# Optimization experiments

Measured on AMD Instinct MI355X. Metric: run time of the kernel, lower is better.

The kernel has to match this reference:

```python
import jax, jax.numpy as jnp
import numpy as np

UNITS = 512
INPUT_SIZE = 512
BATCH = 64
SEQ_LEN = 512


def setup_inputs() -> dict:
    key = jax.random.key(0)
    k_x, k_wx, k_wh = jax.random.split(key, 3)
    scale_x = 1.0 / np.sqrt(INPUT_SIZE)
    scale_h = 1.0 / np.sqrt(UNITS)
    return {
        "x": jax.random.normal(k_x, (BATCH, SEQ_LEN, INPUT_SIZE), dtype=jnp.float32),
        "h0": jnp.zeros((BATCH, UNITS), dtype=jnp.float32),
        "c0": jnp.zeros((BATCH, UNITS), dtype=jnp.float32),
        "Wx": jax.random.normal(k_wx, (INPUT_SIZE, 4 * UNITS), dtype=jnp.float32) * scale_x,
        "Wh": jax.random.normal(k_wh, (UNITS, 4 * UNITS), dtype=jnp.float32) * scale_h,
        "b": jnp.zeros((4 * UNITS,), dtype=jnp.float32),
    }


def reference(x, h0, c0, Wx, Wh, b):
    """LSTM layer over full sequence; returns stacked hidden states [seq_len, batch, units]
    (matching TensorArray.stack() time-major output of the original)."""

    def step(carry, xt):
        h, c = carry
        # fused gate pre-activations: [batch, 4*units]
        z = xt @ Wx + h @ Wh + b
        i, f, g, o = jnp.split(z, 4, axis=-1)  # Keras gate order: i, f, c(g), o
        i = jax.nn.sigmoid(i)
        f = jax.nn.sigmoid(f)
        g = jnp.tanh(g)
        o = jax.nn.sigmoid(o)
        c_new = f * c + i * g
        h_new = o * jnp.tanh(c_new)
        return (h_new, c_new), h_new

    xs = jnp.swapaxes(x, 0, 1)  # [seq_len, batch, input_size]
    (_, _), hs = jax.lax.scan(step, (h0, c0), xs)
    return hs  # [seq_len, batch, units]
```

## Files before the change

### kernel.cpp

```cpp
#include <hip/hip_runtime.h>
#include <stdint.h>


#define OFF_XBF   0ull
#define OFF_HL    33554432ull
#define OFF_HG    33816576ull

typedef short short8 __attribute__((ext_vector_type(8)));
typedef float f32x4 __attribute__((ext_vector_type(4)));
typedef unsigned u32x4 __attribute__((ext_vector_type(4)));

__device__ __forceinline__ unsigned f32_to_bf16(float f) {
    union { float f; unsigned u; } v; v.f = f;
    unsigned u = v.u;
    unsigned r = u + 0x7FFFu + ((u >> 16) & 1u);
    return r >> 16;
}

__global__ void prep_kernel(const float* __restrict__ x,
                            const float* __restrict__ h0,
                            unsigned char* __restrict__ ws) {
    long long i = (long long)blockIdx.x * blockDim.x + threadIdx.x;
    if (i < 2097152) {
        const float4* xs = (const float4*)x + i * 2;
        float4 a = xs[0], b = xs[1];
        unsigned w0 = f32_to_bf16(a.x) | (f32_to_bf16(a.y) << 16);
        unsigned w1 = f32_to_bf16(a.z) | (f32_to_bf16(a.w) << 16);
        unsigned w2 = f32_to_bf16(b.x) | (f32_to_bf16(b.y) << 16);
        unsigned w3 = f32_to_bf16(b.z) | (f32_to_bf16(b.w) << 16);
        uint4 o; o.x = w0; o.y = w1; o.z = w2; o.w = w3;
        ((uint4*)(ws + OFF_XBF))[i] = o;
        return;
    }
    i -= 2097152;
    if (i < 16384) {
        int b = (int)(i >> 8), p = (int)(i & 255);
        unsigned lo = f32_to_bf16(h0[b * 512 + 2 * p]);
        unsigned hi = f32_to_bf16(h0[b * 512 + 2 * p + 1]);
        unsigned long long v =
            (unsigned long long)(lo | (hi << 16)) | (1ull << 32);
        ((unsigned long long*)(ws + OFF_HL))[(long long)b * 256 + p] = v;
        ((unsigned long long*)(ws + OFF_HG))[(long long)b * 256 + p] = v;
    }
}

#define POLL_ONCE(BASEPTR, CPOL, TAGV, OKV, H0V, H1V)                          \
    {                                                                          \
        u32x4 p0, p1, p2, p3;                                                  \
        asm volatile(                                                          \
            "global_load_dwordx4 %0, %4, off " CPOL "\n\t"                     \
            "global_load_dwordx4 %1, %4, off offset:16 " CPOL "\n\t"           \
            "global_load_dwordx4 %2, %4, off offset:32 " CPOL "\n\t"           \
            "global_load_dwordx4 %3, %4, off offset:48 " CPOL "\n\t"           \
            "s_waitcnt vmcnt(0)"                                               \
            : "=v"(p0), "=v"(p1), "=v"(p2), "=v"(p3)                           \
            : "v"(BASEPTR)                                                     \
            : "memory");                                                       \
        unsigned bad = (p0.y ^ (TAGV)) | (p0.w ^ (TAGV))                       \
                     | (p1.y ^ (TAGV)) | (p1.w ^ (TAGV))                       \
                     | (p2.y ^ (TAGV)) | (p2.w ^ (TAGV))                       \
                     | (p3.y ^ (TAGV)) | (p3.w ^ (TAGV));                      \
        OKV = (bad == 0u);                                                     \
        if (OKV) {                                                             \
            H0V.x = p0.x; H0V.y = p0.z; H0V.z = p1.x; H0V.w = p1.z;            \
            H1V.x = p2.x; H1V.y = p2.z; H1V.z = p3.x; H1V.w = p3.z;            \
        }                                                                      \
    }

#define SPIN_DUAL(LPTR, GPTR, TAGV, H0V, H1V)                                  \
    {                                                                          \
        int ok_ = 0, it_ = 0;                                                  \
        for (;;) {                                                             \
            POLL_ONCE(LPTR, "sc0", TAGV, ok_, H0V, H1V);                       \
            if (ok_) break;                                                    \
            if ((it_ & 7) == 7) {                                              \
                POLL_ONCE(GPTR, "sc0 sc1", TAGV, ok_, H0V, H1V);               \
                if (ok_) break;                                                \
            }                                                                  \
            ++it_;                                                             \
            __builtin_amdgcn_s_sleep(0);                                       \
        }                                                                      \
    }

__launch_bounds__(256, 1)
__global__ void lstm_kernel(const float* __restrict__ c0,
                            const float* __restrict__ bias,
                            const float* __restrict__ Wx,
                            const float* __restrict__ Wh,
                            float* __restrict__ out,
                            unsigned char* __restrict__ ws) {
    const int tid  = threadIdx.x;
    const int bid  = blockIdx.x;
    const int s    = bid & 7;
    const int jg   = bid >> 3;
    const int lane = tid & 63;
    const int wave = tid >> 6;
    const int nl   = lane & 15;
    const int q    = lane >> 4;
    const int up   = nl & 3;
    const int g    = nl >> 2;

    const unsigned short* xbf = (const unsigned short*)(ws + OFF_XBF);
    unsigned long long* HuL = (unsigned long long*)(ws + OFF_HL);
    unsigned long long* HuG = (unsigned long long*)(ws + OFF_HG);

    __shared__ __align__(16) unsigned char lds[20736];
    float* lds_out = (float*)(lds + 16640);

    const int ncol = g * 512 + jg * 16 + wave * 4 + up;
    short8 fWh[16], fWx[16];
#pragma unroll
    for (int kt = 0; kt < 16; ++kt) {
        const int k0 = kt * 32 + q * 8;
        short8 vh, vx;
#pragma unroll
        for (int j = 0; j < 8; ++j) {
            vh[j] = (short)f32_to_bf16(Wh[(long long)(k0 + j) * 2048 + ncol]);
            vx[j] = (short)f32_to_bf16(Wx[(long long)(k0 + j) * 2048 + ncol]);
        }
        fWh[kt] = vh; fWx[kt] = vx;
    }

    const int ub = jg * 16 + wave * 4 + up;
    const float bi  = bias[ub];
    const float bf_ = bias[512 + ub];
    const float bg  = bias[1024 + ub];
    const float bo  = bias[1536 + ub];

    float cr[4];
#pragma unroll
    for (int r = 0; r < 4; ++r) {
        const int m = q * 4 + r;
        cr[r] = (q < 2) ? c0[(8 * s + m) * 512 + ub] : 0.f;
    }

    const int sm = tid >> 5, sc = tid & 31;
    const int sb = 8 * s + sm;
    const unsigned* xsrc_base = (const unsigned*)xbf + (long long)sb * 131072 + sc * 8;
    const unsigned char* hl_base = (const unsigned char*)(HuL + sb * 256 + sc * 8);
    const unsigned char* hg_base = (const unsigned char*)(HuG + sb * 256 + sc * 8);
    uint4* xdst = (uint4*)(lds + sm * 1040 + sc * 32);
    uint4* hdst = (uint4*)(lds + 8320 + sm * 1040 + sc * 32);

    const unsigned char* axp = lds + nl * 1040 + q * 16;
    const unsigned char* ahp = lds + 8320 + nl * 1040 + q * 16;
    const short8 zfrag = {0, 0, 0, 0, 0, 0, 0, 0};

    const int gbase = (lane & 0x30) | (lane & 3);
    const int sl0 = gbase, sl1 = gbase | 4, sl2 = gbase | 8, sl3 = gbase | 12;

    uint4 px0 = *(const uint4*)(xsrc_base);
    uint4 px1 = *(const uint4*)(xsrc_base + 4);
    xdst[0] = px0; xdst[1] = px1;
    px0 = *(const uint4*)(xsrc_base + 256);
    px1 = *(const uint4*)(xsrc_base + 256 + 4);
    __syncthreads();

    f32x4 accx;
    {
        f32x4 a0 = {0.f,0.f,0.f,0.f}, a1 = {0.f,0.f,0.f,0.f};
#pragma unroll
        for (int kt = 0; kt < 16; kt += 2) {
            short8 v0 = (nl < 8) ? *(const short8*)(axp + kt * 64) : zfrag;
            short8 v1 = (nl < 8) ? *(const short8*)(axp + kt * 64 + 64) : zfrag;
            a0 = __builtin_amdgcn_mfma_f32_16x16x32_bf16(v0, fWx[kt], a0, 0, 0, 0);
            a1 = __builtin_amdgcn_mfma_f32_16x16x32_bf16(v1, fWx[kt + 1], a1, 0, 0, 0);
        }
        accx = a0 + a1;
    }
    {
        uint4 h0v, h1v;
        SPIN_DUAL(hl_base, hg_base, 1u, h0v, h1v);
        hdst[0] = h0v; hdst[1] = h1v;
    }
    __syncthreads();

    for (int t = 0; t < 512; ++t) {
        const int wb = (t + 1) & 1;

        f32x4 acch;
        {
            f32x4 a0 = {0.f,0.f,0.f,0.f}, a1 = {0.f,0.f,0.f,0.f};
#pragma unroll
            for (int kt = 0; kt < 16; kt += 2) {
                short8 v0 = (nl < 8) ? *(const short8*)(ahp + kt * 64) : zfrag;
                short8 v1 = (nl < 8) ? *(const short8*)(ahp + kt * 64 + 64) : zfrag;
                a0 = __builtin_amdgcn_mfma_f32_16x16x32_bf16(v0, fWh[kt], a0, 0, 0, 0);
                a1 = __builtin_amdgcn_mfma_f32_16x16x32_bf16(v1, fWh[kt + 1], a1, 0, 0, 0);
            }
            acch = a0 + a1;
        }

        float hn[4]; unsigned hb[4];
#pragma unroll
        for (int r = 0; r < 4; ++r) {
            float zs = accx[r] + acch[r];
            float z0 = __shfl(zs, sl0, 64) + bi;
            float z1 = __shfl(zs, sl1, 64) + bf_;
            float z2 = __shfl(zs, sl2, 64) + bg;
            float z3 = __shfl(zs, sl3, 64) + bo;
            float ig = __fdividef(1.f, 1.f + __expf(-z0));
            float fg = __fdividef(1.f, 1.f + __expf(-z1));
            float z2c = fminf(fmaxf(z2, -20.f), 20.f);
            float e2 = __expf(2.f * z2c);
            float gg = __fdividef(e2 - 1.f, e2 + 1.f);
            float og = __fdividef(1.f, 1.f + __expf(-z3));
            float cn = fg * cr[r] + ig * gg;
            cr[r] = cn;
            float cnc = fminf(fmaxf(cn, -20.f), 20.f);
            float ec = __expf(2.f * cnc);
            hn[r] = og * __fdividef(ec - 1.f, ec + 1.f);
            hb[r] = f32_to_bf16(hn[r]);
        }
        unsigned oth[4];
#pragma unroll
        for (int r = 0; r < 4; ++r)
            oth[r] = (unsigned)__shfl((int)hb[r], lane ^ 1, 64);

        if (q < 2 && g == 0) {
#pragma unroll
            for (int r = 0; r < 4; ++r)
                lds_out[(t & 7) * 128 + (q * 4 + r) * 16 + wave * 4 + up] = hn[r];
            if ((up & 1) == 0) {
#pragma unroll
                for (int r = 0; r < 4; ++r) {
                    unsigned long long v = (unsigned long long)(hb[r] | (oth[r] << 16))
                                         | ((unsigned long long)(unsigned)(t + 2) << 32);
                    const size_t idx = (size_t)wb * 16384
                                     + (size_t)(8 * s + q * 4 + r) * 256
                                     + jg * 8 + wave * 2 + (up >> 1);
                    asm volatile("global_store_dwordx2 %0, %1, off sc0"
                                 :: "v"(HuL + idx), "v"(v) : "memory");
                    asm volatile("global_store_dwordx2 %0, %1, off sc0 sc1"
                                 :: "v"(HuG + idx), "v"(v) : "memory");
                }
            }
        }

        xdst[0] = px0; xdst[1] = px1;
        {
            const int tp = (t + 2 < 512) ? (t + 2) : 511;
            px0 = *(const uint4*)(xsrc_base + tp * 256);
            px1 = *(const uint4*)(xsrc_base + tp * 256 + 4);
        }
        __syncthreads();

        if ((t & 7) == 7) {
            const int stp = tid >> 5, brow = (tid >> 2) & 7, qd = tid & 3;
            float4 v = *(const float4*)(lds_out + stp * 128 + brow * 16 + qd * 4);
            *(float4*)(out + (long long)(t - 7 + stp) * 32768
                           + (8 * s + brow) * 512 + jg * 16 + qd * 4) = v;
        }

        {
            f32x4 a0 = {0.f,0.f,0.f,0.f}, a1 = {0.f,0.f,0.f,0.f};
#pragma unroll
            for (int kt = 0; kt < 16; kt += 2) {
                short8 v0 = (nl < 8) ? *(const short8*)(axp + kt * 64) : zfrag;
                short8 v1 = (nl < 8) ? *(const short8*)(axp + kt * 64 + 64) : zfrag;
                a0 = __builtin_amdgcn_mfma_f32_16x16x32_bf16(v0, fWx[kt], a0, 0, 0, 0);
                a1 = __builtin_amdgcn_mfma_f32_16x16x32_bf16(v1, fWx[kt + 1], a1, 0, 0, 0);
            }
            accx = a0 + a1;
        }

        {
            const unsigned char* hl = hl_base + (size_t)wb * 131072;
            const unsigned char* hg = hg_base + (size_t)wb * 131072;
            const unsigned tag = (unsigned)(t + 2);
            uint4 h0v, h1v;
            SPIN_DUAL(hl, hg, tag, h0v, h1v);
            hdst[0] = h0v; hdst[1] = h1v;
        }
        __syncthreads();
    }
}

extern "C" void kernel_launch(void* const* d_in, const int* in_sizes, int n_in,
                              void* d_out, int out_size, void* d_ws, size_t ws_size,
                              hipStream_t stream) {
    const float* x  = (const float*)d_in[0];
    const float* h0 = (const float*)d_in[1];
    const float* c0 = (const float*)d_in[2];
    const float* Wx = (const float*)d_in[3];
    const float* Wh = (const float*)d_in[4];
    const float* b  = (const float*)d_in[5];
    unsigned char* ws = (unsigned char*)d_ws;
    float* out = (float*)d_out;

    const long long n0 = 2097152 + 16384;
    const int blocks0 = (int)((n0 + 255) / 256);
    hipLaunchKernelGGL(prep_kernel, dim3(blocks0), dim3(256), 0, stream, x, h0, ws);
    hipLaunchKernelGGL(lstm_kernel, dim3(256), dim3(256), 0, stream,
                       c0, b, Wx, Wh, out, ws);
}
```

Before: 2.133 ms.

## Assign LSTM work slices by physical XCD via atomic roster

Each block reads its hardware XCC ID and takes a rank through an atomic roster, then waits at a grid-wide barrier. Blocks are mapped to batch slices so that the blocks sharing a slice run on the same XCD, where the polling of h through the local (sc0) cache path can succeed. Blocks beyond 32 per XCD are redistributed to the slots left empty. The change also polls the global coherence path more often (every 4 iterations instead of 8). It adds a startup barrier and relies on all 256 blocks being co-resident.

```diff
diff --git a/kernel.cpp b/kernel.cpp
--- a/kernel.cpp
+++ b/kernel.cpp
@@ -2,9 +2,10 @@
 #include <stdint.h>
 
 
-#define OFF_XBF   0ull
-#define OFF_HL    33554432ull
-#define OFF_HG    33816576ull
+#define OFF_XBF    0ull
+#define OFF_ROSTER 33554432ull
+#define OFF_HL     33558528ull
+#define OFF_HG     33820672ull
 
 typedef short short8 __attribute__((ext_vector_type(8)));
 typedef float f32x4 __attribute__((ext_vector_type(4)));
@@ -41,6 +42,11 @@
             (unsigned long long)(lo | (hi << 16)) | (1ull << 32);
         ((unsigned long long*)(ws + OFF_HL))[(long long)b * 256 + p] = v;
         ((unsigned long long*)(ws + OFF_HG))[(long long)b * 256 + p] = v;
+        return;
+    }
+    i -= 16384;
+    if (i < 16) {
+        ((unsigned*)(ws + OFF_ROSTER))[i] = 0u;
     }
 }
 
@@ -73,7 +79,7 @@
         for (;;) {                                                             \
             POLL_ONCE(LPTR, "sc0", TAGV, ok_, H0V, H1V);                       \
             if (ok_) break;                                                    \
-            if ((it_ & 7) == 7) {                                              \
+            if ((it_ & 3) == 3) {                                              \
                 POLL_ONCE(GPTR, "sc0 sc1", TAGV, ok_, H0V, H1V);               \
                 if (ok_) break;                                                \
             }                                                                  \
@@ -90,15 +96,52 @@
                             float* __restrict__ out,
                             unsigned char* __restrict__ ws) {
     const int tid  = threadIdx.x;
-    const int bid  = blockIdx.x;
-    const int s    = bid & 7;
-    const int jg   = bid >> 3;
     const int lane = tid & 63;
     const int wave = tid >> 6;
     const int nl   = lane & 15;
     const int q    = lane >> 4;
     const int up   = nl & 3;
     const int g    = nl >> 2;
+
+    __shared__ int rsh_s, rsh_jg;
+    if (tid == 0) {
+        unsigned xcd = 0;
+        asm volatile("s_getreg_b32 %0, hwreg(HW_REG_XCC_ID)" : "=s"(xcd));
+        xcd &= 7u;
+        unsigned* R = (unsigned*)(ws + OFF_ROSTER);
+        unsigned rank = __hip_atomic_fetch_add(R + xcd, 1u, __ATOMIC_RELAXED,
+                                               __HIP_MEMORY_SCOPE_AGENT);
+        __hip_atomic_fetch_add(R + 8, 1u, __ATOMIC_RELEASE,
+                               __HIP_MEMORY_SCOPE_AGENT);
+        while (__hip_atomic_load(R + 8, __ATOMIC_ACQUIRE,
+                                 __HIP_MEMORY_SCOPE_AGENT) != 256u)
+            __builtin_amdgcn_s_sleep(8);
+        unsigned cnt[8];
+        for (int x = 0; x < 8; ++x)
+            cnt[x] = __hip_atomic_load(R + x, __ATOMIC_RELAXED,
+                                       __HIP_MEMORY_SCOPE_AGENT);
+        int ss = -1, jj = 0;
+        if (rank < 32u) {
+            ss = (int)xcd; jj = (int)rank;
+        } else {
+            int ov = (int)rank - 32;
+            for (unsigned x = 0; x < xcd; ++x)
+                ov += (cnt[x] > 32u) ? (int)(cnt[x] - 32u) : 0;
+            int k = 0;
+            for (int x = 0; x < 8 && ss < 0; ++x) {
+                int j0 = (cnt[x] < 32u) ? (int)cnt[x] : 32;
+                for (int j = j0; j < 32 && ss < 0; ++j) {
+                    if (k == ov) { ss = x; jj = j; }
+                    ++k;
+                }
+            }
+            if (ss < 0) { ss = 0; jj = 0; }
+        }
+        rsh_s = ss; rsh_jg = jj;
+    }
+    __syncthreads();
+    const int s  = rsh_s;
+    const int jg = rsh_jg;
 
     const unsigned short* xbf = (const unsigned short*)(ws + OFF_XBF);
     unsigned long long* HuL = (unsigned long long*)(ws + OFF_HL);
@@ -288,7 +331,7 @@
     unsigned char* ws = (unsigned char*)d_ws;
     float* out = (float*)d_out;
 
-    const long long n0 = 2097152 + 16384;
+    const long long n0 = 2097152 + 16384 + 16;
     const int blocks0 = (int)((n0 + 255) / 256);
     hipLaunchKernelGGL(prep_kernel, dim3(blocks0), dim3(256), 0, stream, x, h0, ws);
     hipLaunchKernelGGL(lstm_kernel, dim3(256), dim3(256), 0, stream,
```

Result: faster. 1.850 ms (-13.3%).
